# Optimization experiments

Measured on AMD Instinct MI355X. Metric: run time of the kernel, lower is better.

## Reference

```python
import jax, jax.numpy as jnp
import numpy as np

N, E, G = 50000, 640000, 16384
F_IN, H = 128, 128
EPS = 1e-5
_BN_S = 1.0 / np.sqrt(1.0 + EPS)  # BatchNorm1d eval mode: running_mean=0, running_var=1


def _forward(floats, edge_src, edge_dst, game_indices):
    (x, in_bn_g, in_bn_b, lin_W, lin_b, bn0_g, bn0_b,
     cW1, cb1, bn1_g, bn1_b, cW2, cb2, bn2_g, bn2_b, cW3, cb3, bn3_g, bn3_b,
     hW1, hb1, hbn_g, hbn_b, hW2, hb2, hW3, hb3,
     oW1, ob1, obn1_g, obn1_b, oW2, ob2, obn2_g, obn2_b, oW3, ob3) = floats
    n = x.shape[0]

    def bn(z, g, b):  # eval-mode BN with zero running mean, unit running var
        return g * (z * _BN_S) + b

    # GCN symmetric normalization with self-loops: deg_i = 1 + in_degree_i
    deg = jnp.ones((n,), x.dtype).at[edge_dst].add(1.0)
    dis = jax.lax.rsqrt(deg)
    coef = (dis[edge_src] * dis[edge_dst])[:, None]      # [E,1]
    self_coef = (dis * dis)[:, None]                      # [N,1] self-loop weight 1/deg

    def gcn(h, W, b):
        hw = h @ W                                        # [N,H]
        agg = jax.ops.segment_sum(hw[edge_src] * coef, edge_dst, num_segments=n)
        return agg + hw * self_coef + b

    h = bn(x, in_bn_g, in_bn_b)
    h = jax.nn.relu(bn(h @ lin_W + lin_b, bn0_g, bn0_b))
    h = h + jax.nn.relu(bn(gcn(h, cW1, cb1), bn1_g, bn1_b))
    h = h + jax.nn.relu(bn(gcn(h, cW2, cb2), bn2_g, bn2_b))
    h = h + jax.nn.relu(bn(gcn(h, cW3, cb3), bn3_g, bn3_b))

    xg = h[game_indices]                                  # [G,H]
    z = jnp.einsum('gf,hfo->hgo', xg, hW1) + hb1[:, None, :]
    z = jax.nn.relu(hbn_g[:, None, :] * (z * _BN_S) + hbn_b[:, None, :])
    z = jax.nn.relu(jnp.einsum('hgo,hok->hgk', z, hW2) + hb2[:, None, :])
    heads = (jnp.einsum('hgk,hko->hgo', z, hW3) + hb3[:, None, :])[:, :, 0].T  # [G,4]
    # outcome classification head -> [G,3]
    o = jax.nn.relu(bn(xg @ oW1 + ob1, obn1_g, obn1_b))
    o = jax.nn.relu(bn(o @ oW2 + ob2, obn2_g, obn2_b))
    o = o @ oW3 + ob3
    # columns: home_goals, away_goals, home_shots, away_shots, outcome_logits(3)
    return jnp.concatenate([heads, o], axis=-1)          # [G,7]


def setup_inputs() -> dict:
    key = jax.random.key(0)
    ks = iter(jax.random.split(key, 64))
    f32 = jnp.float32

    def rn(shape, s=0.05):
        return jax.random.normal(next(ks), shape, f32) * s

    H2, H4 = H // 2, H // 4
    return {
        'x': jax.random.normal(next(ks), (N, F_IN), f32),
        'edge_src': jax.random.randint(next(ks), (E,), 0, N),
        'edge_dst': jax.random.randint(next(ks), (E,), 0, N),
        'game_indices': jax.random.randint(next(ks), (G,), 0, N),
        'in_bn_g': jnp.ones((F_IN,), f32), 'in_bn_b': jnp.zeros((F_IN,), f32),
        'lin_W': rn((F_IN, H)), 'lin_b': jnp.zeros((H,), f32),
        'bn0_g': jnp.ones((H,), f32), 'bn0_b': jnp.zeros((H,), f32),
        'cW1': rn((H, H)), 'cb1': jnp.zeros((H,), f32),
        'bn1_g': jnp.ones((H,), f32), 'bn1_b': jnp.zeros((H,), f32),
        'cW2': rn((H, H)), 'cb2': jnp.zeros((H,), f32),
        'bn2_g': jnp.ones((H,), f32), 'bn2_b': jnp.zeros((H,), f32),
        'cW3': rn((H, H)), 'cb3': jnp.zeros((H,), f32),
        'bn3_g': jnp.ones((H,), f32), 'bn3_b': jnp.zeros((H,), f32),
        'hW1': rn((4, H, H2)), 'hb1': jnp.zeros((4, H2), f32),
        'hbn_g': jnp.ones((4, H2), f32), 'hbn_b': jnp.zeros((4, H2), f32),
        'hW2': rn((4, H2, H4)), 'hb2': jnp.zeros((4, H4), f32),
        'hW3': rn((4, H4, 1)), 'hb3': jnp.zeros((4, 1), f32),
        'oW1': rn((H, H2)), 'ob1': jnp.zeros((H2,), f32),
        'obn1_g': jnp.ones((H2,), f32), 'obn1_b': jnp.zeros((H2,), f32),
        'oW2': rn((H2, H4)), 'ob2': jnp.zeros((H4,), f32),
        'obn2_g': jnp.ones((H4,), f32), 'obn2_b': jnp.zeros((H4,), f32),
        'oW3': rn((H4, 3)), 'ob3': jnp.zeros((3,), f32),
    }


def reference(x, edge_src, edge_dst, game_indices, in_bn_g, in_bn_b, lin_W, lin_b,
              bn0_g, bn0_b, cW1, cb1, bn1_g, bn1_b, cW2, cb2, bn2_g, bn2_b,
              cW3, cb3, bn3_g, bn3_b, hW1, hb1, hbn_g, hbn_b, hW2, hb2, hW3, hb3,
              oW1, ob1, obn1_g, obn1_b, oW2, ob2, obn2_g, obn2_b, oW3, ob3):
    floats = (x, in_bn_g, in_bn_b, lin_W, lin_b, bn0_g, bn0_b,
              cW1, cb1, bn1_g, bn1_b, cW2, cb2, bn2_g, bn2_b, cW3, cb3, bn3_g, bn3_b,
              hW1, hb1, hbn_g, hbn_b, hW2, hb2, hW3, hb3,
              oW1, ob1, obn1_g, obn1_b, oW2, ob2, obn2_g, obn2_b, oW3, ob3)
    return _forward(floats, edge_src, edge_dst, game_indices)
```

## Files before the change

### kernel.cpp

```cpp
#include <hip/hip_runtime.h>
#include <hip/hip_bf16.h>

#define HDIM 128
#define PAD 64
static constexpr float BN_S = 0.99999500003749968751f;

typedef float f32x4 __attribute__((ext_vector_type(4)));
typedef short s16x8 __attribute__((ext_vector_type(8)));

union U128 { uint4 u; s16x8 s; };

__device__ __forceinline__ unsigned short f2bs(float f){
    union{float f; unsigned u;} c; c.f = f;
    unsigned r = c.u + 0x7fffu + ((c.u >> 16) & 1u);
    return (unsigned short)(r >> 16);
}
__device__ __forceinline__ float bs2f(unsigned short s){
    union{unsigned u; float f;} c; c.u = ((unsigned)s) << 16;
    return c.f;
}
__device__ __forceinline__ float ulo(unsigned u){ union{unsigned i; float f;} c; c.i = u << 16; return c.f; }
__device__ __forceinline__ float uhi(unsigned u){ union{unsigned i; float f;} c; c.i = u & 0xffff0000u; return c.f; }

__global__ __launch_bounds__(256) void k_prep(
    const float* __restrict__ linW, const float* __restrict__ cW1,
    const float* __restrict__ cW2, const float* __restrict__ cW3,
    const float* __restrict__ hW1, const float* __restrict__ oW1,
    const float* __restrict__ hW2, const float* __restrict__ oW2,
    unsigned short* __restrict__ wf, unsigned short* __restrict__ p1,
    unsigned short* __restrict__ p2)
{
    int id = blockIdx.x * 256 + threadIdx.x;
    if (id < 65536){
        int mat = id >> 14;
        int el = id & 16383;
        int k = el >> 7, n = el & 127;
        const float* W = (mat == 0) ? linW : (mat == 1) ? cW1 : (mat == 2) ? cW2 : cW3;
        float v = W[k * 128 + n];
        unsigned short hs = f2bs(v);
        unsigned short ls = f2bs(v - bs2f(hs));
        int nt = n >> 4, lanen = n & 15, kc = k >> 5, quad = (k >> 3) & 3, j = k & 7;
        int lane = quad * 16 + lanen;
        size_t base = (size_t)mat * 32768;
        wf[base + (size_t)(((nt * 4 + kc) * 2 + 0) * 64 + lane) * 8 + j] = hs;
        wf[base + (size_t)(((nt * 4 + kc) * 2 + 1) * 64 + lane) * 8 + j] = ls;
    } else if (id < 65536 + 51200){
        int id1 = id - 65536;
        if (id1 < 40960){
            int j = id1 & 7, lane = (id1 >> 3) & 63, kc = (id1 >> 9) & 3, nt = (id1 >> 11) & 3, y = id1 >> 13;
            int k = kc * 32 + (lane >> 4) * 8 + j;
            int n = nt * 16 + (lane & 15);
            float w = (y < 4) ? hW1[(y * 128 + k) * 64 + n] : oW1[k * 64 + n];
            p1[id1] = f2bs(w);
        } else {
            int id2 = id1 - 40960;
            int j = id2 & 7, lane = (id2 >> 3) & 63, kc = (id2 >> 9) & 1, nt = (id2 >> 10) & 1, y = id2 >> 11;
            int k = kc * 32 + (lane >> 4) * 8 + j;
            int n = nt * 16 + (lane & 15);
            float w = (y < 4) ? hW2[(y * 64 + k) * 32 + n] : oW2[k * 32 + n];
            p2[id2] = f2bs(w);
        }
    }
}

__global__ __launch_bounds__(256) void k_cg01e(
    const float* __restrict__ x, const uint4* __restrict__ wf0, const uint4* __restrict__ wf1,
    const float* __restrict__ ing, const float* __restrict__ inb,
    const float* __restrict__ lb, const float* __restrict__ g0, const float* __restrict__ b0,
    float* __restrict__ hout, unsigned short* __restrict__ hwout, int nrows, int gb,
    const int* __restrict__ esrc, const int* __restrict__ edst,
    int* __restrict__ cnt, unsigned short* __restrict__ slots, int E)
{
    __shared__ __align__(16) unsigned sbuf[64 * 136];
    int bid = blockIdx.x;
    int t = threadIdx.x;

    if (bid >= gb){
        int e = (bid - gb) * 256 + t;
        if (e < E){
            int d = edst[e];
            int r = atomicAdd(&cnt[d], 1);
            if (r < PAD) slots[(size_t)d * PAD + r] = (unsigned short)esrc[e];
        }
        return;
    }

    unsigned* sAhi = sbuf;
    unsigned* sAlo = sbuf + 64 * 68;
    int row0 = bid * 64;
    for (int i = t; i < 2048; i += 256){
        int r = i >> 5, q = i & 31;
        int gr = row0 + r;
        float4 v = make_float4(0.f, 0.f, 0.f, 0.f);
        if (gr < nrows) v = *(const float4*)&x[(size_t)gr * 128 + q * 4];
        float4 g = *(const float4*)&ing[q * 4];
        float4 bo = *(const float4*)&inb[q * 4];
        v.x = v.x * (g.x * BN_S) + bo.x;
        v.y = v.y * (g.y * BN_S) + bo.y;
        v.z = v.z * (g.z * BN_S) + bo.z;
        v.w = v.w * (g.w * BN_S) + bo.w;
        unsigned u0 = __float_as_uint(v.x), u1 = __float_as_uint(v.y);
        unsigned u2 = __float_as_uint(v.z), u3 = __float_as_uint(v.w);
        uint2 hi = make_uint2((u0 >> 16) | (u1 & 0xffff0000u), (u2 >> 16) | (u3 & 0xffff0000u));
        unsigned short l0 = f2bs(v.x - __uint_as_float(u0 & 0xffff0000u));
        unsigned short l1 = f2bs(v.y - __uint_as_float(u1 & 0xffff0000u));
        unsigned short l2 = f2bs(v.z - __uint_as_float(u2 & 0xffff0000u));
        unsigned short l3 = f2bs(v.w - __uint_as_float(u3 & 0xffff0000u));
        uint2 lo = make_uint2((unsigned)l0 | ((unsigned)l1 << 16), (unsigned)l2 | ((unsigned)l3 << 16));
        *(uint2*)&sAhi[r * 68 + q * 2] = hi;
        *(uint2*)&sAlo[r * 68 + q * 2] = lo;
    }
    __syncthreads();

    int w = t >> 6, l = t & 63;
    int lanen = l & 15, quad = l >> 4;
    int mrow = w * 16 + lanen;
    f32x4 acc[8];
#pragma unroll
    for (int i = 0; i < 8; ++i) acc[i] = (f32x4){0.f, 0.f, 0.f, 0.f};

#pragma unroll 1
    for (int kc = 0; kc < 4; ++kc){
        U128 ahi, alo;
        ahi.u = *(const uint4*)&sAhi[mrow * 68 + kc * 16 + quad * 4];
        alo.u = *(const uint4*)&sAlo[mrow * 68 + kc * 16 + quad * 4];
        U128 whi[8];
#pragma unroll
        for (int nt = 0; nt < 8; ++nt)
            whi[nt].u = wf0[((nt * 4 + kc) * 2 + 0) * 64 + l];
#pragma unroll
        for (int nt = 0; nt < 8; ++nt)
            acc[nt] = __builtin_amdgcn_mfma_f32_16x16x32_bf16(ahi.s, whi[nt].s, acc[nt], 0, 0, 0);
#pragma unroll
        for (int nt = 0; nt < 8; ++nt)
            acc[nt] = __builtin_amdgcn_mfma_f32_16x16x32_bf16(alo.s, whi[nt].s, acc[nt], 0, 0, 0);
    }

    __syncthreads();
    float* so = (float*)sbuf;
#pragma unroll
    for (int nt = 0; nt < 8; ++nt){
        int n = nt * 16 + lanen;
        float bias = lb[n], g = g0[n], bo = b0[n];
#pragma unroll
        for (int r = 0; r < 4; ++r){
            int row = w * 16 + quad * 4 + r;
            float v = g * ((acc[nt][r] + bias) * BN_S) + bo;
            so[row * 132 + n] = fmaxf(v, 0.f);
        }
    }
    __syncthreads();
    for (int i = t; i < 2048; i += 256){
        int row = i >> 5, c4 = (i & 31) * 4;
        int grow = row0 + row;
        if (grow < nrows)
            *(float4*)&hout[(size_t)grow * 128 + c4] = *(float4*)&so[row * 132 + c4];
    }

    f32x4 acc2[8];
#pragma unroll
    for (int i = 0; i < 8; ++i) acc2[i] = (f32x4){0.f, 0.f, 0.f, 0.f};
#pragma unroll 1
    for (int kc = 0; kc < 4; ++kc){
        float4 a0 = *(const float4*)&so[mrow * 132 + kc * 32 + quad * 8];
        float4 a1 = *(const float4*)&so[mrow * 132 + kc * 32 + quad * 8 + 4];
        U128 af;
        af.u.x = (unsigned)f2bs(a0.x) | ((unsigned)f2bs(a0.y) << 16);
        af.u.y = (unsigned)f2bs(a0.z) | ((unsigned)f2bs(a0.w) << 16);
        af.u.z = (unsigned)f2bs(a1.x) | ((unsigned)f2bs(a1.y) << 16);
        af.u.w = (unsigned)f2bs(a1.z) | ((unsigned)f2bs(a1.w) << 16);
        U128 wh[8];
#pragma unroll
        for (int nt = 0; nt < 8; ++nt)
            wh[nt].u = wf1[((nt * 4 + kc) * 2 + 0) * 64 + l];
#pragma unroll
        for (int nt = 0; nt < 8; ++nt)
            acc2[nt] = __builtin_amdgcn_mfma_f32_16x16x32_bf16(af.s, wh[nt].s, acc2[nt], 0, 0, 0);
    }
    __syncthreads();
    unsigned short* ss = (unsigned short*)sbuf;
#pragma unroll
    for (int nt = 0; nt < 8; ++nt){
        int n = nt * 16 + lanen;
#pragma unroll
        for (int r = 0; r < 4; ++r){
            int row = w * 16 + quad * 4 + r;
            ss[row * 136 + n] = f2bs(acc2[nt][r]);
        }
    }
    __syncthreads();
    for (int i = t; i < 1024; i += 256){
        int row = i >> 4, c = i & 15;
        int grow = row0 + row;
        if (grow < nrows)
            *(uint4*)&hwout[(size_t)grow * 128 + c * 8] = *(uint4*)&ss[row * 136 + c * 8];
    }
}

__global__ __launch_bounds__(256) void k_gemmb(
    const uint4* __restrict__ hb16, const uint4* __restrict__ wf,
    const int* __restrict__ cnt,
    unsigned short* __restrict__ hwout, int nrows)
{
    __shared__ __align__(16) unsigned sbuf[64 * 68];
    __shared__ float sdis[64];
    int t = threadIdx.x;
    int row0 = blockIdx.x * 64;
    if (t < 64){
        int gr = row0 + t;
        sdis[t] = (gr < nrows) ? rsqrtf(1.0f + (float)cnt[gr]) : 1.0f;
    }
    for (int i = t; i < 1024; i += 256){
        int r = i >> 4, c = i & 15;
        int gr = row0 + r;
        uint4 v = make_uint4(0u, 0u, 0u, 0u);
        if (gr < nrows) v = hb16[(size_t)gr * 16 + c];
        *(uint4*)&sbuf[r * 68 + c * 4] = v;
    }
    __syncthreads();

    int w = t >> 6, l = t & 63;
    int lanen = l & 15, quad = l >> 4;
    int mrow = w * 16 + lanen;
    f32x4 acc[8];
#pragma unroll
    for (int i = 0; i < 8; ++i) acc[i] = (f32x4){0.f, 0.f, 0.f, 0.f};
#pragma unroll 1
    for (int kc = 0; kc < 4; ++kc){
        U128 ah;
        ah.u = *(const uint4*)&sbuf[mrow * 68 + kc * 16 + quad * 4];
        U128 wh[8];
#pragma unroll
        for (int nt = 0; nt < 8; ++nt)
            wh[nt].u = wf[((nt * 4 + kc) * 2 + 0) * 64 + l];
#pragma unroll
        for (int nt = 0; nt < 8; ++nt)
            acc[nt] = __builtin_amdgcn_mfma_f32_16x16x32_bf16(ah.s, wh[nt].s, acc[nt], 0, 0, 0);
    }
    __syncthreads();
    unsigned short* ss = (unsigned short*)sbuf;
#pragma unroll
    for (int nt = 0; nt < 8; ++nt){
        int n = nt * 16 + lanen;
#pragma unroll
        for (int r = 0; r < 4; ++r){
            int row = w * 16 + quad * 4 + r;
            ss[row * 136 + n] = f2bs(acc[nt][r] * sdis[row]);
        }
    }
    __syncthreads();
    for (int i = t; i < 1024; i += 256){
        int row = i >> 4, c = i & 15;
        int grow = row0 + row;
        if (grow < nrows)
            *(uint4*)&hwout[(size_t)grow * 128 + c * 8] = *(uint4*)&ss[row * 136 + c * 8];
    }
}

template<int WRITEH, int SCALESRC>
__device__ __forceinline__ void agg_body(
    const unsigned* __restrict__ hwu, float* __restrict__ h,
    const int* __restrict__ cnt, const unsigned short* __restrict__ slots,
    const float* __restrict__ cb, const float* __restrict__ bg, const float* __restrict__ bb,
    uint4* __restrict__ hb16o, int N)
{
    int row = blockIdx.x * 4 + (threadIdx.x >> 6);
    if (row >= N) return;
    int l = threadIdx.x & 63;
    int sub = l >> 4, cg = l & 15;
    int c0 = cnt[row];
    int c = (c0 > PAD) ? PAD : c0;
    float acc[8];
#pragma unroll
    for (int i = 0; i < 8; ++i) acc[i] = 0.f;
    for (int p = 0; p < c; p += 16){
        int base = p + sub * 4;
        if (base < c){
            uint2 s2 = *(const uint2*)&slots[(size_t)row * PAD + base];
            int s0 = (int)(s2.x & 0xffffu);
            int t1 = (int)(s2.x >> 16);
            int t2 = (int)(s2.y & 0xffffu);
            int t3 = (int)(s2.y >> 16);
            int i1 = (base + 1 < c) ? t1 : s0;
            int i2 = (base + 2 < c) ? t2 : s0;
            int i3 = (base + 3 < c) ? t3 : s0;
            float cf0, cf1, cf2, cf3;
            if (SCALESRC){
                cf0 = rsqrtf(1.0f + (float)cnt[s0]);
                cf1 = (base + 1 < c) ? rsqrtf(1.0f + (float)cnt[i1]) : 0.f;
                cf2 = (base + 2 < c) ? rsqrtf(1.0f + (float)cnt[i2]) : 0.f;
                cf3 = (base + 3 < c) ? rsqrtf(1.0f + (float)cnt[i3]) : 0.f;
            } else {
                cf0 = 1.f;
                cf1 = (base + 1 < c) ? 1.f : 0.f;
                cf2 = (base + 2 < c) ? 1.f : 0.f;
                cf3 = (base + 3 < c) ? 1.f : 0.f;
            }
            uint4 v0 = *(const uint4*)&hwu[(size_t)s0 * 64 + cg * 4];
            uint4 v1 = *(const uint4*)&hwu[(size_t)i1 * 64 + cg * 4];
            uint4 v2 = *(const uint4*)&hwu[(size_t)i2 * 64 + cg * 4];
            uint4 v3 = *(const uint4*)&hwu[(size_t)i3 * 64 + cg * 4];
            acc[0] = fmaf(ulo(v0.x), cf0, acc[0]); acc[1] = fmaf(uhi(v0.x), cf0, acc[1]);
            acc[2] = fmaf(ulo(v0.y), cf0, acc[2]); acc[3] = fmaf(uhi(v0.y), cf0, acc[3]);
            acc[4] = fmaf(ulo(v0.z), cf0, acc[4]); acc[5] = fmaf(uhi(v0.z), cf0, acc[5]);
            acc[6] = fmaf(ulo(v0.w), cf0, acc[6]); acc[7] = fmaf(uhi(v0.w), cf0, acc[7]);
            acc[0] = fmaf(ulo(v1.x), cf1, acc[0]); acc[1] = fmaf(uhi(v1.x), cf1, acc[1]);
            acc[2] = fmaf(ulo(v1.y), cf1, acc[2]); acc[3] = fmaf(uhi(v1.y), cf1, acc[3]);
            acc[4] = fmaf(ulo(v1.z), cf1, acc[4]); acc[5] = fmaf(uhi(v1.z), cf1, acc[5]);
            acc[6] = fmaf(ulo(v1.w), cf1, acc[6]); acc[7] = fmaf(uhi(v1.w), cf1, acc[7]);
            acc[0] = fmaf(ulo(v2.x), cf2, acc[0]); acc[1] = fmaf(uhi(v2.x), cf2, acc[1]);
            acc[2] = fmaf(ulo(v2.y), cf2, acc[2]); acc[3] = fmaf(uhi(v2.y), cf2, acc[3]);
            acc[4] = fmaf(ulo(v2.z), cf2, acc[4]); acc[5] = fmaf(uhi(v2.z), cf2, acc[5]);
            acc[6] = fmaf(ulo(v2.w), cf2, acc[6]); acc[7] = fmaf(uhi(v2.w), cf2, acc[7]);
            acc[0] = fmaf(ulo(v3.x), cf3, acc[0]); acc[1] = fmaf(uhi(v3.x), cf3, acc[1]);
            acc[2] = fmaf(ulo(v3.y), cf3, acc[2]); acc[3] = fmaf(uhi(v3.y), cf3, acc[3]);
            acc[4] = fmaf(ulo(v3.z), cf3, acc[4]); acc[5] = fmaf(uhi(v3.z), cf3, acc[5]);
            acc[6] = fmaf(ulo(v3.w), cf3, acc[6]); acc[7] = fmaf(uhi(v3.w), cf3, acc[7]);
        }
    }
#pragma unroll
    for (int i = 0; i < 8; ++i){
        acc[i] += __shfl_xor(acc[i], 16);
        acc[i] += __shfl_xor(acc[i], 32);
    }
    if (sub == 0){
        float d = rsqrtf(1.0f + (float)c0);
        float selfs = SCALESRC ? d : 1.f;
        uint4 sv = *(const uint4*)&hwu[(size_t)row * 64 + cg * 4];
        float sf[8] = {ulo(sv.x), uhi(sv.x), ulo(sv.y), uhi(sv.y),
                       ulo(sv.z), uhi(sv.z), ulo(sv.w), uhi(sv.w)};
        float4 c0v = *(const float4*)&cb[cg * 8], c1v = *(const float4*)&cb[cg * 8 + 4];
        float4 g0v = *(const float4*)&bg[cg * 8], g1v = *(const float4*)&bg[cg * 8 + 4];
        float4 b0v = *(const float4*)&bb[cg * 8], b1v = *(const float4*)&bb[cg * 8 + 4];
        float cc[8] = {c0v.x, c0v.y, c0v.z, c0v.w, c1v.x, c1v.y, c1v.z, c1v.w};
        float gg[8] = {g0v.x, g0v.y, g0v.z, g0v.w, g1v.x, g1v.y, g1v.z, g1v.w};
        float bo[8] = {b0v.x, b0v.y, b0v.z, b0v.w, b1v.x, b1v.y, b1v.z, b1v.w};
        float4 cur0 = *(const float4*)&h[(size_t)row * 128 + cg * 8];
        float4 cur1 = *(const float4*)&h[(size_t)row * 128 + cg * 8 + 4];
        float o[8] = {cur0.x, cur0.y, cur0.z, cur0.w, cur1.x, cur1.y, cur1.z, cur1.w};
#pragma unroll
        for (int i = 0; i < 8; ++i){
            float v = gg[i] * (((acc[i] + sf[i] * selfs) * d + cc[i]) * BN_S) + bo[i];
            o[i] += fmaxf(v, 0.f);
        }
        if (WRITEH){
            *(float4*)&h[(size_t)row * 128 + cg * 8] = make_float4(o[0], o[1], o[2], o[3]);
            *(float4*)&h[(size_t)row * 128 + cg * 8 + 4] = make_float4(o[4], o[5], o[6], o[7]);
        }
        uint4 pk;
        pk.x = (unsigned)f2bs(o[0]) | ((unsigned)f2bs(o[1]) << 16);
        pk.y = (unsigned)f2bs(o[2]) | ((unsigned)f2bs(o[3]) << 16);
        pk.z = (unsigned)f2bs(o[4]) | ((unsigned)f2bs(o[5]) << 16);
        pk.w = (unsigned)f2bs(o[6]) | ((unsigned)f2bs(o[7]) << 16);
        hb16o[(size_t)row * 16 + cg] = pk;
    }
}

__global__ __launch_bounds__(256) void k_agg1(
    const unsigned* __restrict__ hwu, float* __restrict__ h,
    const int* __restrict__ cnt, const unsigned short* __restrict__ slots,
    const float* __restrict__ cb, const float* __restrict__ bg, const float* __restrict__ bb,
    uint4* __restrict__ hb16o, int N)
{
    agg_body<1, 1>(hwu, h, cnt, slots, cb, bg, bb, hb16o, N);
}

__global__ __launch_bounds__(256) void k_agg(
    const unsigned* __restrict__ hwu, float* __restrict__ h,
    const int* __restrict__ cnt, const unsigned short* __restrict__ slots,
    const float* __restrict__ cb, const float* __restrict__ bg, const float* __restrict__ bb,
    uint4* __restrict__ hb16o, int N)
{
    agg_body<1, 0>(hwu, h, cnt, slots, cb, bg, bb, hb16o, N);
}

__global__ __launch_bounds__(256) void k_agg3(
    const unsigned* __restrict__ hwu, float* __restrict__ h,
    const int* __restrict__ cnt, const unsigned short* __restrict__ slots,
    const float* __restrict__ cb, const float* __restrict__ bg, const float* __restrict__ bb,
    uint4* __restrict__ hb16o, int N)
{
    agg_body<0, 0>(hwu, h, cnt, slots, cb, bg, bb, hb16o, N);
}

__global__ __launch_bounds__(256) void k_headmm(
    const uint4* __restrict__ hb16, const int* __restrict__ gidx,
    const uint4* __restrict__ p1v, const uint4* __restrict__ p2v,
    const float* __restrict__ hb1, const float* __restrict__ hg1, const float* __restrict__ hbb1,
    const float* __restrict__ hb2,
    const float* __restrict__ hW3, const float* __restrict__ hb3,
    const float* __restrict__ ob1, const float* __restrict__ og1, const float* __restrict__ obb1,
    const float* __restrict__ ob2, const float* __restrict__ og2, const float* __restrict__ obb2,
    const float* __restrict__ oW3, const float* __restrict__ ob3,
    float* __restrict__ out, int G)
{
    __shared__ __align__(16) unsigned sxg[64 * 68];
    __shared__ __align__(16) unsigned sz1u[64 * 36];
    __shared__ __align__(16) unsigned sz2u[64 * 20];
    __shared__ float sb1[64], sg1[64], sbb1[64];
    __shared__ float sb2[32], sg2[32], sbb2[32];
    __shared__ float sW3[96];
    __shared__ float sb3[3];
    __shared__ int sgi[64];

    int t = threadIdx.x;
    int gblk = blockIdx.x;
    int y = blockIdx.y;
    bool bn2 = (y == 4);
    int w = t >> 6, l = t & 63;
    int lanen = l & 15, quad = l >> 4;

    const float* b1  = bn2 ? ob1  : (hb1 + y * 64);
    const float* g1  = bn2 ? og1  : (hg1 + y * 64);
    const float* bb1 = bn2 ? obb1 : (hbb1 + y * 64);
    const float* b2  = bn2 ? ob2  : (hb2 + y * 32);
    const float* W3  = bn2 ? oW3  : (hW3 + y * 32);
    const float* b3  = bn2 ? ob3  : (hb3 + y);
    int nc3 = bn2 ? 3 : 1;

    if (t < 64){
        sb1[t] = b1[t]; sg1[t] = g1[t]; sbb1[t] = bb1[t];
        if (t < 3) sb3[t] = (t < nc3) ? b3[t] : 0.f;
    } else if (t < 96){
        int p = t - 64;
        sb2[p] = b2[p];
        sg2[p] = bn2 ? og2[p] : 1.f;
        sbb2[p] = bn2 ? obb2[p] : 0.f;
    } else if (t < 192){
        int i = t - 96;
        sW3[i] = (i < 32 * nc3) ? W3[i] : 0.f;
    } else {
        int r = t - 192;
        int g = gblk * 64 + r;
        sgi[r] = (g < G) ? gidx[g] : 0;
    }
    __syncthreads();
    for (int i = t; i < 1024; i += 256){
        int r = i >> 4, c = i & 15;
        int node = sgi[r];
        uint4 v = hb16[(size_t)node * 16 + c];
        *(uint4*)&sxg[r * 68 + c * 4] = v;
    }
    __syncthreads();

    f32x4 acc1[4] = {{0.f,0.f,0.f,0.f},{0.f,0.f,0.f,0.f},{0.f,0.f,0.f,0.f},{0.f,0.f,0.f,0.f}};
#pragma unroll
    for (int kc = 0; kc < 4; ++kc){
        U128 a;
        a.u = *(const uint4*)&sxg[(w * 16 + lanen) * 68 + kc * 16 + quad * 4];
#pragma unroll
        for (int nt = 0; nt < 4; ++nt){
            U128 bfr;
            bfr.u = p1v[((y * 4 + nt) * 4 + kc) * 64 + l];
            acc1[nt] = __builtin_amdgcn_mfma_f32_16x16x32_bf16(a.s, bfr.s, acc1[nt], 0, 0, 0);
        }
    }
    {
        unsigned short* sz1s = (unsigned short*)sz1u;
#pragma unroll
        for (int nt = 0; nt < 4; ++nt){
            int n = nt * 16 + lanen;
            float g = sg1[n], bia = sb1[n], bt = sbb1[n];
#pragma unroll
            for (int r = 0; r < 4; ++r){
                int row = w * 16 + quad * 4 + r;
                float v = g * ((acc1[nt][r] + bia) * BN_S) + bt;
                sz1s[row * 72 + n] = f2bs(fmaxf(v, 0.f));
            }
        }
    }
    __syncthreads();

    f32x4 acc2[2] = {{0.f,0.f,0.f,0.f},{0.f,0.f,0.f,0.f}};
#pragma unroll
    for (int kc = 0; kc < 2; ++kc){
        U128 a;
        a.u = *(const uint4*)&sz1u[(w * 16 + lanen) * 36 + kc * 16 + quad * 4];
#pragma unroll
        for (int nt = 0; nt < 2; ++nt){
            U128 bfr;
            bfr.u = p2v[((y * 2 + nt) * 2 + kc) * 64 + l];
            acc2[nt] = __builtin_amdgcn_mfma_f32_16x16x32_bf16(a.s, bfr.s, acc2[nt], 0, 0, 0);
        }
    }
    {
        unsigned short* sz2s = (unsigned short*)sz2u;
#pragma unroll
        for (int nt = 0; nt < 2; ++nt){
            int n = nt * 16 + lanen;
            float bia = sb2[n], g = sg2[n], bt = sbb2[n];
#pragma unroll
            for (int r = 0; r < 4; ++r){
                int row = w * 16 + quad * 4 + r;
                float v = acc2[nt][r] + bia;
                if (bn2) v = g * (v * BN_S) + bt;
                sz2s[row * 40 + n] = f2bs(fmaxf(v, 0.f));
            }
        }
    }
    __syncthreads();

    const unsigned short* sz2s = (const unsigned short*)sz2u;
    if (!bn2){
        if (t < 64){
            int g = gblk * 64 + t;
            if (g < G){
                float s = sb3[0];
#pragma unroll
                for (int p = 0; p < 32; ++p) s = fmaf(bs2f(sz2s[t * 40 + p]), sW3[p], s);
                out[(size_t)g * 7 + y] = s;
            }
        }
    } else {
        if (t < 192){
            int gl = t / 3, c = t % 3;
            int g = gblk * 64 + gl;
            if (g < G){
                float s = sb3[c];
#pragma unroll
                for (int p = 0; p < 32; ++p) s = fmaf(bs2f(sz2s[gl * 40 + p]), sW3[p * 3 + c], s);
                out[(size_t)g * 7 + 4 + c] = s;
            }
        }
    }
}

extern "C" void kernel_launch(void* const* d_in, const int* in_sizes, int n_in,
                              void* d_out, int out_size, void* d_ws, size_t ws_size,
                              hipStream_t stream)
{
    const float* x    = (const float*)d_in[0];
    const int* esrc   = (const int*)d_in[1];
    const int* edst   = (const int*)d_in[2];
    const int* gidx   = (const int*)d_in[3];
    const float* in_g = (const float*)d_in[4];
    const float* in_b = (const float*)d_in[5];
    const float* lin_W = (const float*)d_in[6];
    const float* lin_b = (const float*)d_in[7];
    const float* bn0_g = (const float*)d_in[8];
    const float* bn0_b = (const float*)d_in[9];
    const float* cW[3] = {(const float*)d_in[10], (const float*)d_in[14], (const float*)d_in[18]};
    const float* cb[3] = {(const float*)d_in[11], (const float*)d_in[15], (const float*)d_in[19]};
    const float* bg[3] = {(const float*)d_in[12], (const float*)d_in[16], (const float*)d_in[20]};
    const float* bb[3] = {(const float*)d_in[13], (const float*)d_in[17], (const float*)d_in[21]};
    const float* hW1 = (const float*)d_in[22];
    const float* hb1 = (const float*)d_in[23];
    const float* hg1 = (const float*)d_in[24];
    const float* hbb1 = (const float*)d_in[25];
    const float* hW2 = (const float*)d_in[26];
    const float* hb2 = (const float*)d_in[27];
    const float* hW3 = (const float*)d_in[28];
    const float* hb3 = (const float*)d_in[29];
    const float* oW1 = (const float*)d_in[30];
    const float* ob1 = (const float*)d_in[31];
    const float* og1 = (const float*)d_in[32];
    const float* obb1 = (const float*)d_in[33];
    const float* oW2 = (const float*)d_in[34];
    const float* ob2 = (const float*)d_in[35];
    const float* og2 = (const float*)d_in[36];
    const float* obb2 = (const float*)d_in[37];
    const float* oW3 = (const float*)d_in[38];
    const float* ob3 = (const float*)d_in[39];

    const int N = in_sizes[0] / HDIM;
    const int E = in_sizes[1];
    const int G = in_sizes[3];

    char* wsp = (char*)d_ws;
    size_t off = 0;
    auto alloc = [&](size_t bytes) -> char* {
        char* p = wsp + off;
        off = (off + bytes + 255) & ~(size_t)255;
        return p;
    };
    int* cnt      = (int*)alloc((size_t)N * 4);
    unsigned short* slots = (unsigned short*)alloc((size_t)N * PAD * 2);
    float* hbuf   = (float*)alloc((size_t)N * HDIM * 4);
    unsigned short* hwbA = (unsigned short*)alloc((size_t)N * HDIM * 2);
    unsigned short* hwbB = (unsigned short*)alloc((size_t)N * HDIM * 2);
    unsigned short* hb16 = (unsigned short*)alloc((size_t)N * HDIM * 2);
    unsigned short* p1 = (unsigned short*)alloc(40960 * 2);
    unsigned short* p2 = (unsigned short*)alloc(10240 * 2);
    unsigned short* wf = (unsigned short*)alloc((size_t)4 * 32768 * 2);

    int gb = (N + 63) / 64;
    int nCB = (E + 255) / 256;

    hipMemsetAsync(cnt, 0, (size_t)N * 4, stream);
    k_prep<<<dim3((65536 + 51200 + 255) / 256), dim3(256), 0, stream>>>(
        lin_W, cW[0], cW[1], cW[2], hW1, oW1, hW2, oW2, wf, p1, p2);
    k_cg01e<<<dim3(gb + nCB), dim3(256), 0, stream>>>(
        x, (const uint4*)wf, (const uint4*)(wf + (size_t)32768),
        in_g, in_b, lin_b, bn0_g, bn0_b, hbuf, hwbA, N, gb,
        esrc, edst, cnt, slots, E);
    k_agg1<<<dim3((N + 3) / 4), dim3(256), 0, stream>>>(
        (const unsigned*)hwbA, hbuf, cnt, slots, cb[0], bg[0], bb[0], (uint4*)hb16, N);
    k_gemmb<<<dim3(gb), dim3(256), 0, stream>>>(
        (const uint4*)hb16, (const uint4*)(wf + (size_t)2 * 32768), cnt, hwbB, N);
    k_agg<<<dim3((N + 3) / 4), dim3(256), 0, stream>>>(
        (const unsigned*)hwbB, hbuf, cnt, slots, cb[1], bg[1], bb[1], (uint4*)hb16, N);
    k_gemmb<<<dim3(gb), dim3(256), 0, stream>>>(
        (const uint4*)hb16, (const uint4*)(wf + (size_t)3 * 32768), cnt, hwbA, N);
    k_agg3<<<dim3((N + 3) / 4), dim3(256), 0, stream>>>(
        (const unsigned*)hwbA, hbuf, cnt, slots, cb[2], bg[2], bb[2], (uint4*)hb16, N);
    k_headmm<<<dim3((G + 63) / 64, 5), dim3(256), 0, stream>>>(
        (const uint4*)hb16, gidx, (const uint4*)p1, (const uint4*)p2,
        hb1, hg1, hbb1, hb2, hW3, hb3,
        ob1, og1, obb1, ob2, og2, obb2, oW3, ob3,
        (float*)d_out, G);
}
```

Baseline: 316.8 us.

## Split GCN aggregation across four column blocks via a second grid dimension

Each aggregation kernel now launches four times as many blocks, one per 32-column slice of the 128-wide feature row. Each thread gathers one packed bf16 pair per neighbour instead of a 16-byte vector, which cuts per-thread registers and raises parallelism. In exchange, the neighbour slot lists, the degree counts and the rsqrt coefficients are re-read four times. Each gather also becomes a narrower 4-byte load spread across more blocks.

Measured after the change: 444.7 us. +40.4%, slower.

```diff
diff --git a/kernel.cpp b/kernel.cpp
--- a/kernel.cpp
+++ b/kernel.cpp
@@ -262,17 +262,16 @@
     const unsigned* __restrict__ hwu, float* __restrict__ h,
     const int* __restrict__ cnt, const unsigned short* __restrict__ slots,
     const float* __restrict__ cb, const float* __restrict__ bg, const float* __restrict__ bb,
-    uint4* __restrict__ hb16o, int N)
+    unsigned* __restrict__ hb16o, int N)
 {
     int row = blockIdx.x * 4 + (threadIdx.x >> 6);
+    int y = blockIdx.y;
     if (row >= N) return;
     int l = threadIdx.x & 63;
     int sub = l >> 4, cg = l & 15;
     int c0 = cnt[row];
     int c = (c0 > PAD) ? PAD : c0;
-    float acc[8];
-#pragma unroll
-    for (int i = 0; i < 8; ++i) acc[i] = 0.f;
+    float a0 = 0.f, a1 = 0.f;
     for (int p = 0; p < c; p += 16){
         int base = p + sub * 4;
         if (base < c){
@@ -296,63 +295,35 @@
                 cf2 = (base + 2 < c) ? 1.f : 0.f;
                 cf3 = (base + 3 < c) ? 1.f : 0.f;
             }
-            uint4 v0 = *(const uint4*)&hwu[(size_t)s0 * 64 + cg * 4];
-            uint4 v1 = *(const uint4*)&hwu[(size_t)i1 * 64 + cg * 4];
-            uint4 v2 = *(const uint4*)&hwu[(size_t)i2 * 64 + cg * 4];
-            uint4 v3 = *(const uint4*)&hwu[(size_t)i3 * 64 + cg * 4];
-            acc[0] = fmaf(ulo(v0.x), cf0, acc[0]); acc[1] = fmaf(uhi(v0.x), cf0, acc[1]);
-            acc[2] = fmaf(ulo(v0.y), cf0, acc[2]); acc[3] = fmaf(uhi(v0.y), cf0, acc[3]);
-            acc[4] = fmaf(ulo(v0.z), cf0, acc[4]); acc[5] = fmaf(uhi(v0.z), cf0, acc[5]);
-            acc[6] = fmaf(ulo(v0.w), cf0, acc[6]); acc[7] = fmaf(uhi(v0.w), cf0, acc[7]);
-            acc[0] = fmaf(ulo(v1.x), cf1, acc[0]); acc[1] = fmaf(uhi(v1.x), cf1, acc[1]);
-            acc[2] = fmaf(ulo(v1.y), cf1, acc[2]); acc[3] = fmaf(uhi(v1.y), cf1, acc[3]);
-            acc[4] = fmaf(ulo(v1.z), cf1, acc[4]); acc[5] = fmaf(uhi(v1.z), cf1, acc[5]);
-            acc[6] = fmaf(ulo(v1.w), cf1, acc[6]); acc[7] = fmaf(uhi(v1.w), cf1, acc[7]);
-            acc[0] = fmaf(ulo(v2.x), cf2, acc[0]); acc[1] = fmaf(uhi(v2.x), cf2, acc[1]);
-            acc[2] = fmaf(ulo(v2.y), cf2, acc[2]); acc[3] = fmaf(uhi(v2.y), cf2, acc[3]);
-            acc[4] = fmaf(ulo(v2.z), cf2, acc[4]); acc[5] = fmaf(uhi(v2.z), cf2, acc[5]);
-            acc[6] = fmaf(ulo(v2.w), cf2, acc[6]); acc[7] = fmaf(uhi(v2.w), cf2, acc[7]);
-            acc[0] = fmaf(ulo(v3.x), cf3, acc[0]); acc[1] = fmaf(uhi(v3.x), cf3, acc[1]);
-            acc[2] = fmaf(ulo(v3.y), cf3, acc[2]); acc[3] = fmaf(uhi(v3.y), cf3, acc[3]);
-            acc[4] = fmaf(ulo(v3.z), cf3, acc[4]); acc[5] = fmaf(uhi(v3.z), cf3, acc[5]);
-            acc[6] = fmaf(ulo(v3.w), cf3, acc[6]); acc[7] = fmaf(uhi(v3.w), cf3, acc[7]);
-        }
-    }
-#pragma unroll
-    for (int i = 0; i < 8; ++i){
-        acc[i] += __shfl_xor(acc[i], 16);
-        acc[i] += __shfl_xor(acc[i], 32);
-    }
+            unsigned v0 = hwu[(size_t)s0 * 64 + y * 16 + cg];
+            unsigned v1 = hwu[(size_t)i1 * 64 + y * 16 + cg];
+            unsigned v2 = hwu[(size_t)i2 * 64 + y * 16 + cg];
+            unsigned v3 = hwu[(size_t)i3 * 64 + y * 16 + cg];
+            a0 = fmaf(ulo(v0), cf0, a0); a1 = fmaf(uhi(v0), cf0, a1);
+            a0 = fmaf(ulo(v1), cf1, a0); a1 = fmaf(uhi(v1), cf1, a1);
+            a0 = fmaf(ulo(v2), cf2, a0); a1 = fmaf(uhi(v2), cf2, a1);
+            a0 = fmaf(ulo(v3), cf3, a0); a1 = fmaf(uhi(v3), cf3, a1);
+        }
+    }
+    a0 += __shfl_xor(a0, 16); a0 += __shfl_xor(a0, 32);
+    a1 += __shfl_xor(a1, 16); a1 += __shfl_xor(a1, 32);
     if (sub == 0){
         float d = rsqrtf(1.0f + (float)c0);
         float selfs = SCALESRC ? d : 1.f;
-        uint4 sv = *(const uint4*)&hwu[(size_t)row * 64 + cg * 4];
-        float sf[8] = {ulo(sv.x), uhi(sv.x), ulo(sv.y), uhi(sv.y),
-                       ulo(sv.z), uhi(sv.z), ulo(sv.w), uhi(sv.w)};
-        float4 c0v = *(const float4*)&cb[cg * 8], c1v = *(const float4*)&cb[cg * 8 + 4];
-        float4 g0v = *(const float4*)&bg[cg * 8], g1v = *(const float4*)&bg[cg * 8 + 4];
-        float4 b0v = *(const float4*)&bb[cg * 8], b1v = *(const float4*)&bb[cg * 8 + 4];
-        float cc[8] = {c0v.x, c0v.y, c0v.z, c0v.w, c1v.x, c1v.y, c1v.z, c1v.w};
-        float gg[8] = {g0v.x, g0v.y, g0v.z, g0v.w, g1v.x, g1v.y, g1v.z, g1v.w};
-        float bo[8] = {b0v.x, b0v.y, b0v.z, b0v.w, b1v.x, b1v.y, b1v.z, b1v.w};
-        float4 cur0 = *(const float4*)&h[(size_t)row * 128 + cg * 8];
-        float4 cur1 = *(const float4*)&h[(size_t)row * 128 + cg * 8 + 4];
-        float o[8] = {cur0.x, cur0.y, cur0.z, cur0.w, cur1.x, cur1.y, cur1.z, cur1.w};
-#pragma unroll
-        for (int i = 0; i < 8; ++i){
-            float v = gg[i] * (((acc[i] + sf[i] * selfs) * d + cc[i]) * BN_S) + bo[i];
-            o[i] += fmaxf(v, 0.f);
-        }
-        if (WRITEH){
-            *(float4*)&h[(size_t)row * 128 + cg * 8] = make_float4(o[0], o[1], o[2], o[3]);
-            *(float4*)&h[(size_t)row * 128 + cg * 8 + 4] = make_float4(o[4], o[5], o[6], o[7]);
-        }
-        uint4 pk;
-        pk.x = (unsigned)f2bs(o[0]) | ((unsigned)f2bs(o[1]) << 16);
-        pk.y = (unsigned)f2bs(o[2]) | ((unsigned)f2bs(o[3]) << 16);
-        pk.z = (unsigned)f2bs(o[4]) | ((unsigned)f2bs(o[5]) << 16);
-        pk.w = (unsigned)f2bs(o[6]) | ((unsigned)f2bs(o[7]) << 16);
-        hb16o[(size_t)row * 16 + cg] = pk;
+        unsigned sv = hwu[(size_t)row * 64 + y * 16 + cg];
+        int n0 = y * 32 + cg * 2;
+        float2 ccv = *(const float2*)&cb[n0];
+        float2 ggv = *(const float2*)&bg[n0];
+        float2 bov = *(const float2*)&bb[n0];
+        float2 cur = *(const float2*)&h[(size_t)row * 128 + n0];
+        float v0 = ggv.x * (((a0 + ulo(sv) * selfs) * d + ccv.x) * BN_S) + bov.x;
+        float v1 = ggv.y * (((a1 + uhi(sv) * selfs) * d + ccv.y) * BN_S) + bov.y;
+        float o0 = cur.x + fmaxf(v0, 0.f);
+        float o1 = cur.y + fmaxf(v1, 0.f);
+        if (WRITEH)
+            *(float2*)&h[(size_t)row * 128 + n0] = make_float2(o0, o1);
+        hb16o[(size_t)row * 64 + y * 16 + cg] =
+            (unsigned)f2bs(o0) | ((unsigned)f2bs(o1) << 16);
     }
 }
 
@@ -360,7 +331,7 @@
     const unsigned* __restrict__ hwu, float* __restrict__ h,
     const int* __restrict__ cnt, const unsigned short* __restrict__ slots,
     const float* __restrict__ cb, const float* __restrict__ bg, const float* __restrict__ bb,
-    uint4* __restrict__ hb16o, int N)
+    unsigned* __restrict__ hb16o, int N)
 {
     agg_body<1, 1>(hwu, h, cnt, slots, cb, bg, bb, hb16o, N);
 }
@@ -369,7 +340,7 @@
     const unsigned* __restrict__ hwu, float* __restrict__ h,
     const int* __restrict__ cnt, const unsigned short* __restrict__ slots,
     const float* __restrict__ cb, const float* __restrict__ bg, const float* __restrict__ bb,
-    uint4* __restrict__ hb16o, int N)
+    unsigned* __restrict__ hb16o, int N)
 {
     agg_body<1, 0>(hwu, h, cnt, slots, cb, bg, bb, hb16o, N);
 }
@@ -378,7 +349,7 @@
     const unsigned* __restrict__ hwu, float* __restrict__ h,
     const int* __restrict__ cnt, const unsigned short* __restrict__ slots,
     const float* __restrict__ cb, const float* __restrict__ bg, const float* __restrict__ bb,
-    uint4* __restrict__ hb16o, int N)
+    unsigned* __restrict__ hb16o, int N)
 {
     agg_body<0, 0>(hwu, h, cnt, slots, cb, bg, bb, hb16o, N);
 }
@@ -593,16 +564,16 @@
         x, (const uint4*)wf, (const uint4*)(wf + (size_t)32768),
         in_g, in_b, lin_b, bn0_g, bn0_b, hbuf, hwbA, N, gb,
         esrc, edst, cnt, slots, E);
-    k_agg1<<<dim3((N + 3) / 4), dim3(256), 0, stream>>>(
-        (const unsigned*)hwbA, hbuf, cnt, slots, cb[0], bg[0], bb[0], (uint4*)hb16, N);
+    k_agg1<<<dim3((N + 3) / 4, 4), dim3(256), 0, stream>>>(
+        (const unsigned*)hwbA, hbuf, cnt, slots, cb[0], bg[0], bb[0], (unsigned*)hb16, N);
     k_gemmb<<<dim3(gb), dim3(256), 0, stream>>>(
         (const uint4*)hb16, (const uint4*)(wf + (size_t)2 * 32768), cnt, hwbB, N);
-    k_agg<<<dim3((N + 3) / 4), dim3(256), 0, stream>>>(
-        (const unsigned*)hwbB, hbuf, cnt, slots, cb[1], bg[1], bb[1], (uint4*)hb16, N);
+    k_agg<<<dim3((N + 3) / 4, 4), dim3(256), 0, stream>>>(
+        (const unsigned*)hwbB, hbuf, cnt, slots, cb[1], bg[1], bb[1], (unsigned*)hb16, N);
     k_gemmb<<<dim3(gb), dim3(256), 0, stream>>>(
         (const uint4*)hb16, (const uint4*)(wf + (size_t)3 * 32768), cnt, hwbA, N);
-    k_agg3<<<dim3((N + 3) / 4), dim3(256), 0, stream>>>(
-        (const unsigned*)hwbA, hbuf, cnt, slots, cb[2], bg[2], bb[2], (uint4*)hb16, N);
+    k_agg3<<<dim3((N + 3) / 4, 4), dim3(256), 0, stream>>>(
+        (const unsigned*)hwbA, hbuf, cnt, slots, cb[2], bg[2], bb[2], (unsigned*)hb16, N);
     k_headmm<<<dim3((G + 63) / 64, 5), dim3(256), 0, stream>>>(
         (const uint4*)hb16, gidx, (const uint4*)p1, (const uint4*)p2,
         hb1, hg1, hbb1, hb2, hW3, hb3,
```

## Skip final-layer aggregation for nodes not referenced by game indices

Applied to the files above, without the earlier changes.

Marks the nodes used by game_indices in a flag array, built by extra blocks in the first fused kernel. The last GCN aggregation then processes only flagged rows, and the second layer writes fp32 h only for flagged rows, since only those rows feed the final residual. This cuts gather and store traffic in the last layer, at the cost of a larger memset and a flag read per row. G=16384 indices over N=50000 nodes cover at most about a third of the rows, so much of the last layer's work can be skipped.

After: 299.5 us. -5.4%, faster.

```diff
diff --git a/kernel.cpp b/kernel.cpp
--- a/kernel.cpp
+++ b/kernel.cpp
@@ -67,20 +67,27 @@
     const float* __restrict__ x, const uint4* __restrict__ wf0, const uint4* __restrict__ wf1,
     const float* __restrict__ ing, const float* __restrict__ inb,
     const float* __restrict__ lb, const float* __restrict__ g0, const float* __restrict__ b0,
-    float* __restrict__ hout, unsigned short* __restrict__ hwout, int nrows, int gb,
+    float* __restrict__ hout, unsigned short* __restrict__ hwout, int nrows, int gb, int nCB,
     const int* __restrict__ esrc, const int* __restrict__ edst,
-    int* __restrict__ cnt, unsigned short* __restrict__ slots, int E)
+    int* __restrict__ cnt, unsigned short* __restrict__ slots, int E,
+    const int* __restrict__ gidx, int* __restrict__ flag, int G)
 {
     __shared__ __align__(16) unsigned sbuf[64 * 136];
     int bid = blockIdx.x;
     int t = threadIdx.x;
 
     if (bid >= gb){
-        int e = (bid - gb) * 256 + t;
-        if (e < E){
-            int d = edst[e];
-            int r = atomicAdd(&cnt[d], 1);
-            if (r < PAD) slots[(size_t)d * PAD + r] = (unsigned short)esrc[e];
+        int cb = bid - gb;
+        if (cb < nCB){
+            int e = cb * 256 + t;
+            if (e < E){
+                int d = edst[e];
+                int r = atomicAdd(&cnt[d], 1);
+                if (r < PAD) slots[(size_t)d * PAD + r] = (unsigned short)esrc[e];
+            }
+        } else {
+            int i = (cb - nCB) * 256 + t;
+            if (i < G) flag[gidx[i]] = 1;
         }
         return;
     }
@@ -257,15 +264,16 @@
     }
 }
 
-template<int WRITEH, int SCALESRC>
+template<int WRITEH, int SCALESRC, int FLAGMODE>
 __device__ __forceinline__ void agg_body(
     const unsigned* __restrict__ hwu, float* __restrict__ h,
     const int* __restrict__ cnt, const unsigned short* __restrict__ slots,
     const float* __restrict__ cb, const float* __restrict__ bg, const float* __restrict__ bb,
-    uint4* __restrict__ hb16o, int N)
+    uint4* __restrict__ hb16o, const int* __restrict__ flag, int N)
 {
     int row = blockIdx.x * 4 + (threadIdx.x >> 6);
     if (row >= N) return;
+    if (FLAGMODE == 2 && flag[row] == 0) return;
     int l = threadIdx.x & 63;
     int sub = l >> 4, cg = l & 15;
     int c0 = cnt[row];
@@ -344,8 +352,11 @@
             o[i] += fmaxf(v, 0.f);
         }
         if (WRITEH){
-            *(float4*)&h[(size_t)row * 128 + cg * 8] = make_float4(o[0], o[1], o[2], o[3]);
-            *(float4*)&h[(size_t)row * 128 + cg * 8 + 4] = make_float4(o[4], o[5], o[6], o[7]);
+            bool wr = (FLAGMODE != 1) || (flag[row] != 0);
+            if (wr){
+                *(float4*)&h[(size_t)row * 128 + cg * 8] = make_float4(o[0], o[1], o[2], o[3]);
+                *(float4*)&h[(size_t)row * 128 + cg * 8 + 4] = make_float4(o[4], o[5], o[6], o[7]);
+            }
         }
         uint4 pk;
         pk.x = (unsigned)f2bs(o[0]) | ((unsigned)f2bs(o[1]) << 16);
@@ -360,27 +371,27 @@
     const unsigned* __restrict__ hwu, float* __restrict__ h,
     const int* __restrict__ cnt, const unsigned short* __restrict__ slots,
     const float* __restrict__ cb, const float* __restrict__ bg, const float* __restrict__ bb,
-    uint4* __restrict__ hb16o, int N)
-{
-    agg_body<1, 1>(hwu, h, cnt, slots, cb, bg, bb, hb16o, N);
-}
-
-__global__ __launch_bounds__(256) void k_agg(
+    uint4* __restrict__ hb16o, const int* __restrict__ flag, int N)
+{
+    agg_body<1, 1, 0>(hwu, h, cnt, slots, cb, bg, bb, hb16o, flag, N);
+}
+
+__global__ __launch_bounds__(256) void k_agg2(
     const unsigned* __restrict__ hwu, float* __restrict__ h,
     const int* __restrict__ cnt, const unsigned short* __restrict__ slots,
     const float* __restrict__ cb, const float* __restrict__ bg, const float* __restrict__ bb,
-    uint4* __restrict__ hb16o, int N)
-{
-    agg_body<1, 0>(hwu, h, cnt, slots, cb, bg, bb, hb16o, N);
+    uint4* __restrict__ hb16o, const int* __restrict__ flag, int N)
+{
+    agg_body<1, 0, 1>(hwu, h, cnt, slots, cb, bg, bb, hb16o, flag, N);
 }
 
 __global__ __launch_bounds__(256) void k_agg3(
     const unsigned* __restrict__ hwu, float* __restrict__ h,
     const int* __restrict__ cnt, const unsigned short* __restrict__ slots,
     const float* __restrict__ cb, const float* __restrict__ bg, const float* __restrict__ bb,
-    uint4* __restrict__ hb16o, int N)
-{
-    agg_body<0, 0>(hwu, h, cnt, slots, cb, bg, bb, hb16o, N);
+    uint4* __restrict__ hb16o, const int* __restrict__ flag, int N)
+{
+    agg_body<0, 0, 2>(hwu, h, cnt, slots, cb, bg, bb, hb16o, flag, N);
 }
 
 __global__ __launch_bounds__(256) void k_headmm(
@@ -573,7 +584,8 @@
         off = (off + bytes + 255) & ~(size_t)255;
         return p;
     };
-    int* cnt      = (int*)alloc((size_t)N * 4);
+    int* cnt      = (int*)alloc((size_t)(2 * N) * 4);
+    int* flag     = cnt + N;
     unsigned short* slots = (unsigned short*)alloc((size_t)N * PAD * 2);
     float* hbuf   = (float*)alloc((size_t)N * HDIM * 4);
     unsigned short* hwbA = (unsigned short*)alloc((size_t)N * HDIM * 2);
@@ -585,24 +597,25 @@
 
     int gb = (N + 63) / 64;
     int nCB = (E + 255) / 256;
-
-    hipMemsetAsync(cnt, 0, (size_t)N * 4, stream);
+    int nFB = (G + 255) / 256;
+
+    hipMemsetAsync(cnt, 0, (size_t)(2 * N) * 4, stream);
     k_prep<<<dim3((65536 + 51200 + 255) / 256), dim3(256), 0, stream>>>(
         lin_W, cW[0], cW[1], cW[2], hW1, oW1, hW2, oW2, wf, p1, p2);
-    k_cg01e<<<dim3(gb + nCB), dim3(256), 0, stream>>>(
+    k_cg01e<<<dim3(gb + nCB + nFB), dim3(256), 0, stream>>>(
         x, (const uint4*)wf, (const uint4*)(wf + (size_t)32768),
-        in_g, in_b, lin_b, bn0_g, bn0_b, hbuf, hwbA, N, gb,
-        esrc, edst, cnt, slots, E);
+        in_g, in_b, lin_b, bn0_g, bn0_b, hbuf, hwbA, N, gb, nCB,
+        esrc, edst, cnt, slots, E, gidx, flag, G);
     k_agg1<<<dim3((N + 3) / 4), dim3(256), 0, stream>>>(
-        (const unsigned*)hwbA, hbuf, cnt, slots, cb[0], bg[0], bb[0], (uint4*)hb16, N);
+        (const unsigned*)hwbA, hbuf, cnt, slots, cb[0], bg[0], bb[0], (uint4*)hb16, flag, N);
     k_gemmb<<<dim3(gb), dim3(256), 0, stream>>>(
         (const uint4*)hb16, (const uint4*)(wf + (size_t)2 * 32768), cnt, hwbB, N);
-    k_agg<<<dim3((N + 3) / 4), dim3(256), 0, stream>>>(
-        (const unsigned*)hwbB, hbuf, cnt, slots, cb[1], bg[1], bb[1], (uint4*)hb16, N);
+    k_agg2<<<dim3((N + 3) / 4), dim3(256), 0, stream>>>(
+        (const unsigned*)hwbB, hbuf, cnt, slots, cb[1], bg[1], bb[1], (uint4*)hb16, flag, N);
     k_gemmb<<<dim3(gb), dim3(256), 0, stream>>>(
         (const uint4*)hb16, (const uint4*)(wf + (size_t)3 * 32768), cnt, hwbA, N);
     k_agg3<<<dim3((N + 3) / 4), dim3(256), 0, stream>>>(
-        (const unsigned*)hwbA, hbuf, cnt, slots, cb[2], bg[2], bb[2], (uint4*)hb16, N);
+        (const unsigned*)hwbA, hbuf, cnt, slots, cb[2], bg[2], bb[2], (uint4*)hb16, flag, N);
     k_headmm<<<dim3((G + 63) / 64, 5), dim3(256), 0, stream>>>(
         (const uint4*)hb16, gidx, (const uint4*)p1, (const uint4*)p2,
         hb1, hg1, hbb1, hb2, hW3, hb3,
```
